# Performance work log

Measured on AMD Instinct MI355X. Metric: run time of the kernel, lower is better.

## Reference

```python
import jax, jax.numpy as jnp
import numpy as np

N_NODES = 100000
N_EDGES = 3200000
NUM_TYPES = 8
TYPE_DIM = 16
IN_DIM = 5
HID = 64
HEADS = 2
OUT = 64
LN_EPS = 1e-5
NEG_SLOPE = 0.2


def segment_softmax(logits, seg, num_segments):
    # logits: [E, H], seg: [E] destination ids
    m = jax.ops.segment_max(logits, seg, num_segments=num_segments)
    m = jnp.where(jnp.isfinite(m), m, 0.0)
    e = jnp.exp(logits - m[seg])
    s = jax.ops.segment_sum(e, seg, num_segments=num_segments)
    return e / (s[seg] + 1e-16)


def gat_conv(x, W, a_src, a_dst, b, src, dst, n_nodes, heads, ch):
    # x: [N, F_in], W: [F_in, heads*ch], a_src/a_dst: [heads, ch], b: [heads*ch]
    h = (x @ W).reshape(n_nodes, heads, ch)            # [N, H, C]
    al_s = jnp.einsum('nhc,hc->nh', h, a_src)          # [N, H]
    al_d = jnp.einsum('nhc,hc->nh', h, a_dst)          # [N, H]
    e = jax.nn.leaky_relu(al_s[src] + al_d[dst], NEG_SLOPE)  # [E, H]
    alpha = segment_softmax(e, dst, n_nodes)           # [E, H]
    msg = alpha[:, :, None] * h[src]                   # [E, H, C]
    out = jax.ops.segment_sum(msg, dst, num_segments=n_nodes)  # [N, H, C]
    return out.reshape(n_nodes, heads * ch) + b


def setup_inputs() -> dict:
    key = jax.random.key(0)
    ks = jax.random.split(key, 16)
    in1 = IN_DIM + TYPE_DIM  # 21
    inp = {
        'x': jax.random.normal(ks[0], (N_NODES, IN_DIM), dtype=jnp.float32),
        'edge_index': jax.random.randint(ks[1], (2, N_EDGES), 0, N_NODES, dtype=jnp.int32),
        'type_ids': jax.random.randint(ks[2], (N_NODES,), 0, NUM_TYPES, dtype=jnp.int32),
        'type_emb': jax.random.normal(ks[3], (NUM_TYPES, TYPE_DIM), dtype=jnp.float32) * 0.3,
        'W1': jax.random.normal(ks[4], (in1, HID), dtype=jnp.float32) * (1.0 / np.sqrt(in1)),
        'a_src1': jax.random.normal(ks[5], (HEADS, HID // HEADS), dtype=jnp.float32) * 0.1,
        'a_dst1': jax.random.normal(ks[6], (HEADS, HID // HEADS), dtype=jnp.float32) * 0.1,
        'b1': jnp.zeros((HID,), dtype=jnp.float32),
        'W2': jax.random.normal(ks[7], (HID, OUT), dtype=jnp.float32) * (1.0 / np.sqrt(HID)),
        'a_src2': jax.random.normal(ks[8], (1, OUT), dtype=jnp.float32) * 0.1,
        'a_dst2': jax.random.normal(ks[9], (1, OUT), dtype=jnp.float32) * 0.1,
        'b2': jnp.zeros((OUT,), dtype=jnp.float32),
        'gamma': jnp.ones((OUT,), dtype=jnp.float32),
        'beta': jnp.zeros((OUT,), dtype=jnp.float32),
    }
    return inp


def reference(x, type_emb, W1, a_src1, a_dst1, b1, W2, a_src2, a_dst2, b2, gamma, beta, edge_index, type_ids):
    n = x.shape[0]
    # type embedding concat
    xin = jnp.concatenate([x, type_emb[type_ids]], axis=1)  # [N, 21]
    # add self loops (PyG GATConv default)
    loops = jnp.arange(n, dtype=edge_index.dtype)
    src = jnp.concatenate([edge_index[0], loops])
    dst = jnp.concatenate([edge_index[1], loops])
    h = gat_conv(xin, W1, a_src1, a_dst1, b1, src, dst, n, HEADS, HID // HEADS)
    h = jax.nn.relu(h)  # dropout = identity at inference
    h = gat_conv(h, W2, a_src2, a_dst2, b2, src, dst, n, 1, OUT)
    # LayerNorm
    mu = jnp.mean(h, axis=-1, keepdims=True)
    var = jnp.var(h, axis=-1, keepdims=True)
    return (h - mu) / jnp.sqrt(var + LN_EPS) * gamma + beta
```

## Files before the change

### kernel.cpp

```cpp
#include <hip/hip_runtime.h>
#include <hip/hip_fp16.h>

#define NEG_SLOPE 0.2f
#define INVLN2 1.44269504088896f
#define BKT_SHIFT 7
#define BKT_NODES 128
#define BKT_CAP 5120
#define SRC_SHIFT 18
#define SRC_MASK 0x3FFFF
#define CHUNK 4096
#define NBMAX 1024

typedef _Float16 half8 __attribute__((ext_vector_type(8)));
typedef float float4v __attribute__((ext_vector_type(4)));

__global__ void k_bucketA(const int* __restrict__ ei, unsigned int* __restrict__ pk,
                          int* __restrict__ bcnt, int E, int NBKT)
{
    __shared__ unsigned int stage[CHUNK];
    __shared__ unsigned short stageB[CHUNK];
    __shared__ int cnt[NBMAX];
    __shared__ int excl[NBMAX];
    __shared__ int curp[NBMAX];
    __shared__ int gbase[NBMAX];

    int t = threadIdx.x;
    int e0 = blockIdx.x * CHUNK;
    bool vec4 = ((E & 3) == 0);

    for (int i = t; i < NBMAX; i += 256) cnt[i] = 0;
    __syncthreads();

    int4 s4[4], d4[4];
    bool val[4];

    if (vec4) {
#pragma unroll
        for (int it = 0; it < 4; it++) {
            int e = e0 + it * 1024 + t * 4;
            val[it] = (e < E);
            if (val[it]) {
                s4[it] = *(const int4*)(ei + e);
                d4[it] = *(const int4*)(ei + (size_t)E + e);
                atomicAdd(&cnt[d4[it].x >> BKT_SHIFT], 1);
                atomicAdd(&cnt[d4[it].y >> BKT_SHIFT], 1);
                atomicAdd(&cnt[d4[it].z >> BKT_SHIFT], 1);
                atomicAdd(&cnt[d4[it].w >> BKT_SHIFT], 1);
            }
        }
    } else {
        for (int i = t; i < CHUNK; i += 256) {
            int e = e0 + i;
            if (e >= E) break;
            atomicAdd(&cnt[ei[E + e] >> BKT_SHIFT], 1);
        }
    }
    __syncthreads();
    for (int i = t; i < NBMAX; i += 256) curp[i] = cnt[i];
    __syncthreads();
    for (int off = 1; off < NBMAX; off <<= 1) {
        int v0 = (t       >= off) ? cnt[t       - off] : 0;
        int v1 = (t + 256 >= off) ? cnt[t + 256 - off] : 0;
        int v2 = (t + 512 >= off) ? cnt[t + 512 - off] : 0;
        int v3 = (t + 768 >= off) ? cnt[t + 768 - off] : 0;
        __syncthreads();
        cnt[t] += v0; cnt[t + 256] += v1; cnt[t + 512] += v2; cnt[t + 768] += v3;
        __syncthreads();
    }
    for (int i = t; i < NBMAX; i += 256) {
        int o = curp[i];
        int ex = cnt[i] - o;
        excl[i] = ex;
        curp[i] = ex;
    }
    __syncthreads();
    for (int b = t; b < NBKT; b += 256) {
        int c = cnt[b] - excl[b];
        gbase[b] = (c > 0) ? atomicAdd(&bcnt[b], c) : 0;
    }
    __syncthreads();
    if (vec4) {
#pragma unroll
        for (int it = 0; it < 4; it++) {
            if (!val[it]) continue;
            int ss[4] = {s4[it].x, s4[it].y, s4[it].z, s4[it].w};
            int dd[4] = {d4[it].x, d4[it].y, d4[it].z, d4[it].w};
#pragma unroll
            for (int k = 0; k < 4; k++) {
                int b = dd[k] >> BKT_SHIFT;
                int p = atomicAdd(&curp[b], 1);
                stage[p] = (unsigned)ss[k] | ((unsigned)(dd[k] & (BKT_NODES - 1)) << SRC_SHIFT);
                stageB[p] = (unsigned short)b;
            }
        }
    } else {
        for (int i = t; i < CHUNK; i += 256) {
            int e = e0 + i;
            if (e >= E) break;
            int s = ei[e], d = ei[E + e];
            int b = d >> BKT_SHIFT;
            int p = atomicAdd(&curp[b], 1);
            stage[p] = (unsigned)s | ((unsigned)(d & (BKT_NODES - 1)) << SRC_SHIFT);
            stageB[p] = (unsigned short)b;
        }
    }
    __syncthreads();
    int total = E - e0; if (total > CHUNK) total = CHUNK;
    for (int i = t; i < total; i += 256) {
        int b = stageB[i];
        int idx = gbase[b] + (i - excl[b]);
        if (idx < BKT_CAP) pk[(size_t)b * BKT_CAP + idx] = stage[i];
    }
}

__global__ __launch_bounds__(256) void k_build_node1(
        const unsigned int* __restrict__ pk, const int* __restrict__ bcnt,
        int* __restrict__ rs, int* __restrict__ cur, int* __restrict__ ssrc,
        const float* __restrict__ x, const int* __restrict__ type_ids,
        const float* __restrict__ type_emb, const float* __restrict__ W1,
        const float* __restrict__ a_src1, const float* __restrict__ a_dst1,
        __half2* __restrict__ h1h, float* __restrict__ als1, float* __restrict__ ald1,
        int N, int NBKT)
{
    __shared__ unsigned int vals[BKT_CAP];
    __shared__ int cnt[BKT_NODES];
    __shared__ int cursor[BKT_NODES];
    __shared__ int orig[BKT_NODES];
    __shared__ int red[256];
    int t = threadIdx.x;

    if (blockIdx.x >= NBKT) {
        int node = (blockIdx.x - NBKT) * 4 + (t >> 6);
        int j = t & 63;
        if (node >= N) return;

        float xin[21];
#pragma unroll
        for (int k = 0; k < 5; k++) xin[k] = x[node * 5 + k];
        int ty = type_ids[node];
#pragma unroll
        for (int k = 0; k < 16; k++) xin[5 + k] = type_emb[ty * 16 + k];

        float h = 0.f;
#pragma unroll
        for (int k = 0; k < 21; k++) h += xin[k] * W1[k * 64 + j];

        float hn = __shfl_xor(h, 1);
        if ((j & 1) == 0)
            h1h[node * 32 + (j >> 1)] = __floats2half2_rn(h, hn);

        int head = j >> 5, lane = j & 31;
        float ps = h * a_src1[head * 32 + lane];
        float pd = h * a_dst1[head * 32 + lane];
#pragma unroll
        for (int m = 16; m >= 1; m >>= 1) { ps += __shfl_xor(ps, m); pd += __shfl_xor(pd, m); }
        if (lane == 0) {
            als1[node * 2 + head] = ps * INVLN2;
            ald1[node * 2 + head] = pd * INVLN2;
        }
        return;
    }

    int b = blockIdx.x;
    int nb = min(bcnt[b], BKT_CAP);

    int part = 0;
    for (int i = t; i < b; i += 256) part += min(bcnt[i], BKT_CAP);
    red[t] = part;
    if (t < BKT_NODES) cnt[t] = 0;
    __syncthreads();
    for (int off = 128; off; off >>= 1) {
        if (t < off) red[t] += red[t + off];
        __syncthreads();
    }
    int bs = red[0];

    const unsigned int* mypk = pk + (size_t)b * BKT_CAP;
    int nb4 = nb & ~3;
    for (int e = t * 4; e < nb4; e += 1024) {
        uint4 v = *(const uint4*)(mypk + e);
        *(uint4*)(vals + e) = v;
        atomicAdd(&cnt[v.x >> SRC_SHIFT], 1);
        atomicAdd(&cnt[v.y >> SRC_SHIFT], 1);
        atomicAdd(&cnt[v.z >> SRC_SHIFT], 1);
        atomicAdd(&cnt[v.w >> SRC_SHIFT], 1);
    }
    for (int e = nb4 + t; e < nb; e += 256) {
        unsigned int v = mypk[e];
        vals[e] = v;
        atomicAdd(&cnt[v >> SRC_SHIFT], 1);
    }
    __syncthreads();
    if (t < BKT_NODES) orig[t] = cnt[t];
    __syncthreads();
    for (int off = 1; off < BKT_NODES; off <<= 1) {
        int v = 0;
        if (t < BKT_NODES && t >= off) v = cnt[t - off];
        __syncthreads();
        if (t < BKT_NODES) cnt[t] += v;
        __syncthreads();
    }
    if (t < BKT_NODES) {
        int c = orig[t];
        int ex = cnt[t] - c;
        cursor[t] = ex;
        int node = (b << BKT_SHIFT) + t;
        if (node < N) { rs[node] = bs + ex; cur[node] = bs + ex + c; }
    }
    __syncthreads();
    for (int e = t; e < nb; e += 256) {
        unsigned int w = vals[e];
        int p = atomicAdd(&cursor[w >> SRC_SHIFT], 1);
        ssrc[bs + p] = (int)(w & SRC_MASK);
    }
}

__global__ void k_gather1(const int* __restrict__ rs, const int* __restrict__ cur,
                          const int* __restrict__ ssrc, const float4* __restrict__ h4,
                          const float* __restrict__ als1, const float* __restrict__ ald1,
                          const float* __restrict__ b1, float4* __restrict__ h2h4, int N)
{
    __shared__ int    sS[4][64];
    __shared__ float2 sW[4][64];
    int wv = threadIdx.x >> 6;
    int node = blockIdx.x * 4 + wv;
    if (node >= N) return;
    int l = threadIdx.x & 63;
    int eg = l >> 3;
    int ch = l & 7;
    int head = ch >> 2;
    float2 ad = ((const float2*)ald1)[node];

    int beg = rs[node], end = cur[node];
    int cnt = end - beg;
    const int* sp = ssrc + beg;
    __half2 acc2[4];
    acc2[0] = acc2[1] = acc2[2] = acc2[3] = __float2half2_rn(0.f);
    float ws0 = 0.f, ws1 = 0.f;

    for (int base = 0; base < cnt; base += 64) {
        int e = base + l;
        bool v = e < cnt;
        int s = v ? sp[e] : node;
        float2 al = ((const float2*)als1)[s];
        float lg0 = al.x + ad.x; lg0 = (lg0 >= 0.f) ? lg0 : NEG_SLOPE * lg0;
        float lg1 = al.y + ad.y; lg1 = (lg1 >= 0.f) ? lg1 : NEG_SLOPE * lg1;
        float w0 = v ? exp2f(lg0) : 0.f;
        float w1 = v ? exp2f(lg1) : 0.f;
        sS[wv][l] = s;
        sW[wv][l] = make_float2(w0, w1);
        ws0 += w0; ws1 += w1;

        int rem = cnt - base;
        const float* sWf = (const float*)&sW[wv][0];
        for (int sub = 0; sub < 8 && sub * 8 < rem; sub += 2) {
            int i0 = sub * 8 + eg, i1 = i0 + 8;
            int sA = sS[wv][i0];
            int sB = sS[wv][i1];
            float wA = sWf[i0 * 2 + head];
            float wB = sWf[i1 * 2 + head];
            float4 rA = h4[(size_t)sA * 8 + ch];
            float4 rB = h4[(size_t)sB * 8 + ch];
            __half2 whA = __float2half2_rn(wA);
            __half2 whB = __float2half2_rn(wB);
            const __half2* pA = (const __half2*)&rA;
            const __half2* pB = (const __half2*)&rB;
#pragma unroll
            for (int q = 0; q < 4; q++) {
                acc2[q] = __hfma2(pA[q], whA, acc2[q]);
                acc2[q] = __hfma2(pB[q], whB, acc2[q]);
            }
        }
    }
    float acc[8];
#pragma unroll
    for (int q = 0; q < 4; q++) {
        float2 f = __half22float2(acc2[q]);
        acc[2*q] = f.x; acc[2*q+1] = f.y;
    }
#pragma unroll
    for (int m = 1; m <= 32; m <<= 1) { ws0 += __shfl_xor(ws0, m); ws1 += __shfl_xor(ws1, m); }
#pragma unroll
    for (int m = 8; m <= 32; m <<= 1) {
#pragma unroll
        for (int q = 0; q < 8; q++) acc[q] += __shfl_xor(acc[q], m);
    }
    float wsum = head ? ws1 : ws0;
    {
        float2 al = ((const float2*)als1)[node];
        float lg = (head ? al.y + ad.y : al.x + ad.x);
        lg = (lg >= 0.f) ? lg : NEG_SLOPE * lg;
        float w = exp2f(lg);
        float4 r = h4[(size_t)node * 8 + ch];
        const __half2* p = (const __half2*)&r;
#pragma unroll
        for (int q = 0; q < 4; q++) {
            float2 f = __half22float2(p[q]);
            acc[2*q] += w * f.x; acc[2*q+1] += w * f.y;
        }
        wsum += w;
    }
    float inv = 1.f / (wsum + 1e-16f);
    if (eg == 0) {
        union { float4 f4; __half2 h2[4]; } u;
#pragma unroll
        for (int q = 0; q < 4; q++) {
            float v0 = fmaxf(acc[2*q]   * inv + b1[ch * 8 + 2*q],     0.f);
            float v1 = fmaxf(acc[2*q+1] * inv + b1[ch * 8 + 2*q + 1], 0.f);
            u.h2[q] = __floats2half2_rn(v0, v1);
        }
        h2h4[(size_t)node * 8 + ch] = u.f4;
    }
}

__global__ __launch_bounds__(256) void k_node2m(
        const _Float16* __restrict__ h2h, const float* __restrict__ W2,
        const float* __restrict__ a_src2, const float* __restrict__ a_dst2,
        _Float16* __restrict__ h3h, float* __restrict__ als2, float* __restrict__ ald2, int N)
{
    __shared__ _Float16 w2t[64][72];
    __shared__ float h3t[4][16][65];
    int t = threadIdx.x;
    for (int e = t; e < 4096; e += 256) {
        int k = e >> 6, n = e & 63;
        w2t[n][k] = (_Float16)W2[e];
    }
    __syncthreads();

    int w = t >> 6, l = t & 63;
    int l15 = l & 15, quad = l >> 4;
    int nodebase = blockIdx.x * 64 + w * 16;

    int arow = nodebase + l15;
    if (arow >= N) arow = N - 1;
    const half8* ap = (const half8*)(h2h + (size_t)arow * 64 + quad * 8);
    half8 a0 = ap[0];
    half8 a1 = ap[4];
    float4v accs[4];
#pragma unroll
    for (int nt = 0; nt < 4; nt++) {
        half8 b0 = *(const half8*)(&w2t[nt * 16 + l15][quad * 8]);
        half8 b1 = *(const half8*)(&w2t[nt * 16 + l15][32 + quad * 8]);
        float4v c = {0.f, 0.f, 0.f, 0.f};
        c = __builtin_amdgcn_mfma_f32_16x16x32_f16(a0, b0, c, 0, 0, 0);
        c = __builtin_amdgcn_mfma_f32_16x16x32_f16(a1, b1, c, 0, 0, 0);
        accs[nt] = c;
    }
#pragma unroll
    for (int nt = 0; nt < 4; nt++)
#pragma unroll
        for (int r = 0; r < 4; r++)
            h3t[w][quad * 4 + r][nt * 16 + l15] = accs[nt][r];
    __syncthreads();

    int m = l >> 2, part = l & 3;
    int g = blockIdx.x * 64 + w * 16 + m;
    float ps = 0.f, pd = 0.f;
    union { float4 f4[2]; _Float16 h[16]; } u;
#pragma unroll
    for (int c = 0; c < 16; c++) {
        float v = h3t[w][m][part * 16 + c];
        ps += v * a_src2[part * 16 + c];
        pd += v * a_dst2[part * 16 + c];
        u.h[c] = (_Float16)v;
    }
    if (g < N) {
        float4* dst = (float4*)(h3h + (size_t)g * 64) + part * 2;
        dst[0] = u.f4[0];
        dst[1] = u.f4[1];
    }
    ps += __shfl_xor(ps, 1); ps += __shfl_xor(ps, 2);
    pd += __shfl_xor(pd, 1); pd += __shfl_xor(pd, 2);
    if (part == 0 && g < N) { als2[g] = ps * INVLN2; ald2[g] = pd * INVLN2; }
}

__global__ void k_gather2(const int* __restrict__ rs, const int* __restrict__ cur,
                          const int* __restrict__ ssrc, const float4* __restrict__ h4,
                          const float* __restrict__ als2, const float* __restrict__ ald2,
                          const float* __restrict__ b2, const float* __restrict__ gamma,
                          const float* __restrict__ beta, float* __restrict__ out, int N)
{
    __shared__ int   sS[4][64];
    __shared__ float sW[4][64];
    int wv = threadIdx.x >> 6;
    int node = blockIdx.x * 4 + wv;
    if (node >= N) return;
    int l = threadIdx.x & 63;
    int eg = l >> 3;
    int ch = l & 7;
    float ad = ald2[node];

    int beg = rs[node], end = cur[node];
    int cnt = end - beg;
    const int* sp = ssrc + beg;
    __half2 acc2[4];
    acc2[0] = acc2[1] = acc2[2] = acc2[3] = __float2half2_rn(0.f);
    float ws = 0.f;

    for (int base = 0; base < cnt; base += 64) {
        int e = base + l;
        bool v = e < cnt;
        int s = v ? sp[e] : node;
        float lg = als2[s] + ad; lg = (lg >= 0.f) ? lg : NEG_SLOPE * lg;
        float w = v ? exp2f(lg) : 0.f;
        sS[wv][l] = s;
        sW[wv][l] = w;
        ws += w;

        int rem = cnt - base;
        for (int sub = 0; sub < 8 && sub * 8 < rem; sub += 2) {
            int i0 = sub * 8 + eg, i1 = i0 + 8;
            int sA = sS[wv][i0];
            int sB = sS[wv][i1];
            float wA = sW[wv][i0];
            float wB = sW[wv][i1];
            float4 rA = h4[(size_t)sA * 8 + ch];
            float4 rB = h4[(size_t)sB * 8 + ch];
            __half2 whA = __float2half2_rn(wA);
            __half2 whB = __float2half2_rn(wB);
            const __half2* pA = (const __half2*)&rA;
            const __half2* pB = (const __half2*)&rB;
#pragma unroll
            for (int q = 0; q < 4; q++) {
                acc2[q] = __hfma2(pA[q], whA, acc2[q]);
                acc2[q] = __hfma2(pB[q], whB, acc2[q]);
            }
        }
    }
    float acc[8];
#pragma unroll
    for (int q = 0; q < 4; q++) {
        float2 f = __half22float2(acc2[q]);
        acc[2*q] = f.x; acc[2*q+1] = f.y;
    }
#pragma unroll
    for (int m = 1; m <= 32; m <<= 1) ws += __shfl_xor(ws, m);
#pragma unroll
    for (int m = 8; m <= 32; m <<= 1) {
#pragma unroll
        for (int q = 0; q < 8; q++) acc[q] += __shfl_xor(acc[q], m);
    }
    {
        float lg = als2[node] + ad;
        lg = (lg >= 0.f) ? lg : NEG_SLOPE * lg;
        float w = exp2f(lg);
        float4 r = h4[(size_t)node * 8 + ch];
        const __half2* p = (const __half2*)&r;
#pragma unroll
        for (int q = 0; q < 4; q++) {
            float2 f = __half22float2(p[q]);
            acc[2*q] += w * f.x; acc[2*q+1] += w * f.y;
        }
        ws += w;
    }
    float inv = 1.f / (ws + 1e-16f);
    float o[8];
    float s = 0.f;
#pragma unroll
    for (int q = 0; q < 8; q++) { o[q] = acc[q] * inv + b2[ch * 8 + q]; s += o[q]; }
#pragma unroll
    for (int m = 1; m <= 4; m <<= 1) s += __shfl_xor(s, m);
    float mu = s * (1.f / 64.f);
    float v = 0.f;
#pragma unroll
    for (int q = 0; q < 8; q++) { float d = o[q] - mu; v += d * d; }
#pragma unroll
    for (int m = 1; m <= 4; m <<= 1) v += __shfl_xor(v, m);
    v *= (1.f / 64.f);
    float r = rsqrtf(v + 1e-5f);
    if (eg == 0) {
        float res[8];
#pragma unroll
        for (int q = 0; q < 8; q++)
            res[q] = (o[q] - mu) * r * gamma[ch * 8 + q] + beta[ch * 8 + q];
        float4* op = (float4*)(out + (size_t)node * 64 + ch * 8);
        op[0] = make_float4(res[0], res[1], res[2], res[3]);
        op[1] = make_float4(res[4], res[5], res[6], res[7]);
    }
}

extern "C" void kernel_launch(void* const* d_in, const int* in_sizes, int n_in,
                              void* d_out, int out_size, void* d_ws, size_t ws_size,
                              hipStream_t stream) {
    const float* x        = (const float*)d_in[0];
    const int*   ei       = (const int*)  d_in[1];
    const int*   type_ids = (const int*)  d_in[2];
    const float* type_emb = (const float*)d_in[3];
    const float* W1       = (const float*)d_in[4];
    const float* a_src1   = (const float*)d_in[5];
    const float* a_dst1   = (const float*)d_in[6];
    const float* b1       = (const float*)d_in[7];
    const float* W2       = (const float*)d_in[8];
    const float* a_src2   = (const float*)d_in[9];
    const float* a_dst2   = (const float*)d_in[10];
    const float* b2       = (const float*)d_in[11];
    const float* gamma    = (const float*)d_in[12];
    const float* beta     = (const float*)d_in[13];

    int N = in_sizes[0] / 5;
    int E = in_sizes[1] / 2;
    int NBKT = (N + BKT_NODES - 1) >> BKT_SHIFT;

    char* base = (char*)d_ws;
    size_t off = 0;
    auto carve = [&](size_t bytes) { void* p = base + off; off += (bytes + 255) & ~(size_t)255; return p; };
    __half2* h1h = (__half2*)carve((size_t)N * 64 * sizeof(__half));
    size_t pk_bytes = (size_t)NBKT * BKT_CAP * sizeof(unsigned int);
    size_t h23_bytes = 2 * (size_t)N * 64 * sizeof(__half);
    char* uni = (char*)carve(pk_bytes > h23_bytes ? pk_bytes : h23_bytes);
    _Float16* h2h = (_Float16*)uni;
    _Float16* h3h = (_Float16*)(uni + (size_t)N * 64 * sizeof(__half));
    unsigned int* pk = (unsigned int*)uni;
    float* als1  = (float*)carve((size_t)N * 2 * sizeof(float));
    float* ald1  = (float*)carve((size_t)N * 2 * sizeof(float));
    float* als2  = (float*)carve((size_t)N * sizeof(float));
    float* ald2  = (float*)carve((size_t)N * sizeof(float));
    int*   rs    = (int*)carve((size_t)N * sizeof(int));
    int*   cur   = (int*)carve((size_t)N * sizeof(int));
    int*   bcnt  = (int*)carve(1024 * sizeof(int));
    int*   ssrc  = (int*)carve((size_t)E * sizeof(int));

    dim3 tb(256);
    dim3 nb((N + 3) / 4);
    int nodeBlocks = (N + 3) / 4;

    hipMemsetAsync(bcnt, 0, NBKT * sizeof(int), stream);
    k_bucketA<<<dim3((E + CHUNK - 1) / CHUNK), tb, 0, stream>>>(ei, pk, bcnt, E, NBKT);

    k_build_node1<<<dim3(NBKT + nodeBlocks), tb, 0, stream>>>(
        pk, bcnt, rs, cur, ssrc,
        x, type_ids, type_emb, W1, a_src1, a_dst1, h1h, als1, ald1,
        N, NBKT);

    k_gather1<<<nb, tb, 0, stream>>>(rs, cur, ssrc, (const float4*)h1h, als1, ald1, b1,
                                     (float4*)h2h, N);
    k_node2m<<<dim3((N + 63) / 64), tb, 0, stream>>>(h2h, W2, a_src2, a_dst2,
                                                     h3h, als2, ald2, N);
    k_gather2<<<nb, tb, 0, stream>>>(rs, cur, ssrc, (const float4*)h3h, als2, ald2, b2,
                                     gamma, beta, (float*)d_out, N);
}
```

Baseline: 326.6 us.

## Split feature gathers into four channel-group planes for cache-resident gathers

Node feature tables are stored as four channel-group planes of 16 halves (32 bytes) each. Each gather kernel is launched with four blocks per node group, one per plane, so every gather pass works on a 3.2 MB working set that fits in L2, and each edge read fetches 32 bytes from one plane. LayerNorm moves into a separate kernel that reads a half-precision intermediate, because no single block now holds a full output row. In exchange, the edge index list and attention logits are reread four times, and there is an extra launch plus an intermediate round trip.

```diff
diff --git a/kernel.cpp b/kernel.cpp
--- a/kernel.cpp
+++ b/kernel.cpp
@@ -13,6 +13,12 @@
 
 typedef _Float16 half8 __attribute__((ext_vector_type(8)));
 typedef float float4v __attribute__((ext_vector_type(4)));
+
+static __device__ __forceinline__ __half2 shfl_xor_h2(__half2 v, int m) {
+    union { __half2 h; int i; } u; u.h = v;
+    u.i = __shfl_xor(u.i, m);
+    return u.h;
+}
 
 __global__ void k_bucketA(const int* __restrict__ ei, unsigned int* __restrict__ pk,
                           int* __restrict__ bcnt, int E, int NBKT)
@@ -119,7 +125,7 @@
         const float* __restrict__ x, const int* __restrict__ type_ids,
         const float* __restrict__ type_emb, const float* __restrict__ W1,
         const float* __restrict__ a_src1, const float* __restrict__ a_dst1,
-        __half2* __restrict__ h1h, float* __restrict__ als1, float* __restrict__ ald1,
+        __half2* __restrict__ h1t, float* __restrict__ als1, float* __restrict__ ald1,
         int N, int NBKT)
 {
     __shared__ unsigned int vals[BKT_CAP];
@@ -146,8 +152,11 @@
         for (int k = 0; k < 21; k++) h += xin[k] * W1[k * 64 + j];
 
         float hn = __shfl_xor(h, 1);
-        if ((j & 1) == 0)
-            h1h[node * 32 + (j >> 1)] = __floats2half2_rn(h, hn);
+        if ((j & 1) == 0) {
+            int g = j >> 4;
+            int idx = (j & 15) >> 1;
+            h1t[((size_t)g * N + node) * 8 + idx] = __floats2half2_rn(h, hn);
+        }
 
         int head = j >> 5, lane = j & 31;
         float ps = h * a_src1[head * 32 + lane];
@@ -215,101 +224,73 @@
     }
 }
 
-__global__ void k_gather1(const int* __restrict__ rs, const int* __restrict__ cur,
-                          const int* __restrict__ ssrc, const float4* __restrict__ h4,
-                          const float* __restrict__ als1, const float* __restrict__ ald1,
-                          const float* __restrict__ b1, float4* __restrict__ h2h4, int N)
+__global__ __launch_bounds__(256) void k_gatherg1(
+        const int* __restrict__ rs, const int* __restrict__ cur,
+        const int* __restrict__ ssrc, const float4* __restrict__ h1t,
+        const float* __restrict__ als1, const float* __restrict__ ald1,
+        const float* __restrict__ b1, float4* __restrict__ h2t, int N)
 {
-    __shared__ int    sS[4][64];
-    __shared__ float2 sW[4][64];
-    int wv = threadIdx.x >> 6;
-    int node = blockIdx.x * 4 + wv;
+    int g = blockIdx.x & 3;
+    int node = (blockIdx.x >> 2) * 4 + (threadIdx.x >> 6);
     if (node >= N) return;
     int l = threadIdx.x & 63;
-    int eg = l >> 3;
-    int ch = l & 7;
-    int head = ch >> 2;
-    float2 ad = ((const float2*)ald1)[node];
-
-    int beg = rs[node], end = cur[node];
-    int cnt = end - beg;
+    int eg = l >> 1, hf = l & 1;
+    int head = g >> 1;
+    float ad = ald1[node * 2 + head];
+
+    int beg = rs[node], cnt = cur[node] - beg;
     const int* sp = ssrc + beg;
     __half2 acc2[4];
     acc2[0] = acc2[1] = acc2[2] = acc2[3] = __float2half2_rn(0.f);
-    float ws0 = 0.f, ws1 = 0.f;
-
-    for (int base = 0; base < cnt; base += 64) {
-        int e = base + l;
+    float ws = 0.f;
+
+    for (int base = 0; base < cnt; base += 32) {
+        int e = base + eg;
         bool v = e < cnt;
         int s = v ? sp[e] : node;
-        float2 al = ((const float2*)als1)[s];
-        float lg0 = al.x + ad.x; lg0 = (lg0 >= 0.f) ? lg0 : NEG_SLOPE * lg0;
-        float lg1 = al.y + ad.y; lg1 = (lg1 >= 0.f) ? lg1 : NEG_SLOPE * lg1;
-        float w0 = v ? exp2f(lg0) : 0.f;
-        float w1 = v ? exp2f(lg1) : 0.f;
-        sS[wv][l] = s;
-        sW[wv][l] = make_float2(w0, w1);
-        ws0 += w0; ws1 += w1;
-
-        int rem = cnt - base;
-        const float* sWf = (const float*)&sW[wv][0];
-        for (int sub = 0; sub < 8 && sub * 8 < rem; sub += 2) {
-            int i0 = sub * 8 + eg, i1 = i0 + 8;
-            int sA = sS[wv][i0];
-            int sB = sS[wv][i1];
-            float wA = sWf[i0 * 2 + head];
-            float wB = sWf[i1 * 2 + head];
-            float4 rA = h4[(size_t)sA * 8 + ch];
-            float4 rB = h4[(size_t)sB * 8 + ch];
-            __half2 whA = __float2half2_rn(wA);
-            __half2 whB = __float2half2_rn(wB);
-            const __half2* pA = (const __half2*)&rA;
-            const __half2* pB = (const __half2*)&rB;
-#pragma unroll
-            for (int q = 0; q < 4; q++) {
-                acc2[q] = __hfma2(pA[q], whA, acc2[q]);
-                acc2[q] = __hfma2(pB[q], whB, acc2[q]);
-            }
-        }
-    }
+        float lg = als1[s * 2 + head] + ad;
+        lg = (lg >= 0.f) ? lg : NEG_SLOPE * lg;
+        float w = v ? exp2f(lg) : 0.f;
+        ws += w;
+        float4 r = h1t[((size_t)g * N + s) * 2 + hf];
+        __half2 wh = __float2half2_rn(w);
+        const __half2* p = (const __half2*)&r;
+#pragma unroll
+        for (int q = 0; q < 4; q++) acc2[q] = __hfma2(p[q], wh, acc2[q]);
+    }
+#pragma unroll
+    for (int m = 2; m <= 32; m <<= 1) {
+#pragma unroll
+        for (int q = 0; q < 4; q++) acc2[q] = __hadd2(acc2[q], shfl_xor_h2(acc2[q], m));
+    }
+#pragma unroll
+    for (int m = 1; m <= 32; m <<= 1) ws += __shfl_xor(ws, m);
+    ws *= 0.5f;
+
     float acc[8];
 #pragma unroll
-    for (int q = 0; q < 4; q++) {
-        float2 f = __half22float2(acc2[q]);
-        acc[2*q] = f.x; acc[2*q+1] = f.y;
-    }
-#pragma unroll
-    for (int m = 1; m <= 32; m <<= 1) { ws0 += __shfl_xor(ws0, m); ws1 += __shfl_xor(ws1, m); }
-#pragma unroll
-    for (int m = 8; m <= 32; m <<= 1) {
-#pragma unroll
-        for (int q = 0; q < 8; q++) acc[q] += __shfl_xor(acc[q], m);
-    }
-    float wsum = head ? ws1 : ws0;
+    for (int q = 0; q < 4; q++) { float2 f = __half22float2(acc2[q]); acc[2*q] = f.x; acc[2*q+1] = f.y; }
     {
-        float2 al = ((const float2*)als1)[node];
-        float lg = (head ? al.y + ad.y : al.x + ad.x);
+        float lg = als1[node * 2 + head] + ad;
         lg = (lg >= 0.f) ? lg : NEG_SLOPE * lg;
         float w = exp2f(lg);
-        float4 r = h4[(size_t)node * 8 + ch];
+        float4 r = h1t[((size_t)g * N + node) * 2 + hf];
         const __half2* p = (const __half2*)&r;
 #pragma unroll
+        for (int q = 0; q < 4; q++) { float2 f = __half22float2(p[q]); acc[2*q] += w * f.x; acc[2*q+1] += w * f.y; }
+        ws += w;
+    }
+    float inv = 1.f / (ws + 1e-16f);
+    if (eg == 0) {
+        const float* bb = b1 + g * 16 + hf * 8;
+        union { float4 f4; __half2 h2[4]; } u;
+#pragma unroll
         for (int q = 0; q < 4; q++) {
-            float2 f = __half22float2(p[q]);
-            acc[2*q] += w * f.x; acc[2*q+1] += w * f.y;
-        }
-        wsum += w;
-    }
-    float inv = 1.f / (wsum + 1e-16f);
-    if (eg == 0) {
-        union { float4 f4; __half2 h2[4]; } u;
-#pragma unroll
-        for (int q = 0; q < 4; q++) {
-            float v0 = fmaxf(acc[2*q]   * inv + b1[ch * 8 + 2*q],     0.f);
-            float v1 = fmaxf(acc[2*q+1] * inv + b1[ch * 8 + 2*q + 1], 0.f);
+            float v0 = fmaxf(acc[2*q]     * inv + bb[2*q],     0.f);
+            float v1 = fmaxf(acc[2*q + 1] * inv + bb[2*q + 1], 0.f);
             u.h2[q] = __floats2half2_rn(v0, v1);
         }
-        h2h4[(size_t)node * 8 + ch] = u.f4;
+        h2t[((size_t)g * N + node) * 2 + hf] = u.f4;
     }
 }
 
@@ -333,9 +314,10 @@
 
     int arow = nodebase + l15;
     if (arow >= N) arow = N - 1;
-    const half8* ap = (const half8*)(h2h + (size_t)arow * 64 + quad * 8);
-    half8 a0 = ap[0];
-    half8 a1 = ap[4];
+    const float4* h2t4 = (const float4*)h2h;
+    int g0 = quad >> 1, hf0 = quad & 1;
+    half8 a0 = *(const half8*)(h2t4 + ((size_t)g0 * N + arow) * 2 + hf0);
+    half8 a1 = *(const half8*)(h2t4 + ((size_t)(g0 + 2) * N + arow) * 2 + hf0);
     float4v accs[4];
 #pragma unroll
     for (int nt = 0; nt < 4; nt++) {
@@ -365,7 +347,7 @@
         u.h[c] = (_Float16)v;
     }
     if (g < N) {
-        float4* dst = (float4*)(h3h + (size_t)g * 64) + part * 2;
+        float4* dst = (float4*)h3h + ((size_t)part * N + g) * 2;
         dst[0] = u.f4[0];
         dst[1] = u.f4[1];
     }
@@ -374,109 +356,89 @@
     if (part == 0 && g < N) { als2[g] = ps * INVLN2; ald2[g] = pd * INVLN2; }
 }
 
-__global__ void k_gather2(const int* __restrict__ rs, const int* __restrict__ cur,
-                          const int* __restrict__ ssrc, const float4* __restrict__ h4,
-                          const float* __restrict__ als2, const float* __restrict__ ald2,
-                          const float* __restrict__ b2, const float* __restrict__ gamma,
-                          const float* __restrict__ beta, float* __restrict__ out, int N)
+__global__ __launch_bounds__(256) void k_gatherg2(
+        const int* __restrict__ rs, const int* __restrict__ cur,
+        const int* __restrict__ ssrc, const float4* __restrict__ h3t,
+        const float* __restrict__ als2, const float* __restrict__ ald2,
+        const float* __restrict__ b2, __half* __restrict__ ot, int N)
 {
-    __shared__ int   sS[4][64];
-    __shared__ float sW[4][64];
-    int wv = threadIdx.x >> 6;
-    int node = blockIdx.x * 4 + wv;
+    int g = blockIdx.x & 3;
+    int node = (blockIdx.x >> 2) * 4 + (threadIdx.x >> 6);
     if (node >= N) return;
     int l = threadIdx.x & 63;
-    int eg = l >> 3;
-    int ch = l & 7;
+    int eg = l >> 1, hf = l & 1;
     float ad = ald2[node];
 
-    int beg = rs[node], end = cur[node];
-    int cnt = end - beg;
+    int beg = rs[node], cnt = cur[node] - beg;
     const int* sp = ssrc + beg;
     __half2 acc2[4];
     acc2[0] = acc2[1] = acc2[2] = acc2[3] = __float2half2_rn(0.f);
     float ws = 0.f;
 
-    for (int base = 0; base < cnt; base += 64) {
-        int e = base + l;
+    for (int base = 0; base < cnt; base += 32) {
+        int e = base + eg;
         bool v = e < cnt;
         int s = v ? sp[e] : node;
-        float lg = als2[s] + ad; lg = (lg >= 0.f) ? lg : NEG_SLOPE * lg;
+        float lg = als2[s] + ad;
+        lg = (lg >= 0.f) ? lg : NEG_SLOPE * lg;
         float w = v ? exp2f(lg) : 0.f;
-        sS[wv][l] = s;
-        sW[wv][l] = w;
         ws += w;
-
-        int rem = cnt - base;
-        for (int sub = 0; sub < 8 && sub * 8 < rem; sub += 2) {
-            int i0 = sub * 8 + eg, i1 = i0 + 8;
-            int sA = sS[wv][i0];
-            int sB = sS[wv][i1];
-            float wA = sW[wv][i0];
-            float wB = sW[wv][i1];
-            float4 rA = h4[(size_t)sA * 8 + ch];
-            float4 rB = h4[(size_t)sB * 8 + ch];
-            __half2 whA = __float2half2_rn(wA);
-            __half2 whB = __float2half2_rn(wB);
-            const __half2* pA = (const __half2*)&rA;
-            const __half2* pB = (const __half2*)&rB;
-#pragma unroll
-            for (int q = 0; q < 4; q++) {
-                acc2[q] = __hfma2(pA[q], whA, acc2[q]);
-                acc2[q] = __hfma2(pB[q], whB, acc2[q]);
-            }
-        }
-    }
+        float4 r = h3t[((size_t)g * N + s) * 2 + hf];
+        __half2 wh = __float2half2_rn(w);
+        const __half2* p = (const __half2*)&r;
+#pragma unroll
+        for (int q = 0; q < 4; q++) acc2[q] = __hfma2(p[q], wh, acc2[q]);
+    }
+#pragma unroll
+    for (int m = 2; m <= 32; m <<= 1) {
+#pragma unroll
+        for (int q = 0; q < 4; q++) acc2[q] = __hadd2(acc2[q], shfl_xor_h2(acc2[q], m));
+    }
+#pragma unroll
+    for (int m = 1; m <= 32; m <<= 1) ws += __shfl_xor(ws, m);
+    ws *= 0.5f;
+
     float acc[8];
 #pragma unroll
-    for (int q = 0; q < 4; q++) {
-        float2 f = __half22float2(acc2[q]);
-        acc[2*q] = f.x; acc[2*q+1] = f.y;
-    }
-#pragma unroll
-    for (int m = 1; m <= 32; m <<= 1) ws += __shfl_xor(ws, m);
-#pragma unroll
-    for (int m = 8; m <= 32; m <<= 1) {
-#pragma unroll
-        for (int q = 0; q < 8; q++) acc[q] += __shfl_xor(acc[q], m);
-    }
+    for (int q = 0; q < 4; q++) { float2 f = __half22float2(acc2[q]); acc[2*q] = f.x; acc[2*q+1] = f.y; }
     {
         float lg = als2[node] + ad;
         lg = (lg >= 0.f) ? lg : NEG_SLOPE * lg;
         float w = exp2f(lg);
-        float4 r = h4[(size_t)node * 8 + ch];
+        float4 r = h3t[((size_t)g * N + node) * 2 + hf];
         const __half2* p = (const __half2*)&r;
 #pragma unroll
-        for (int q = 0; q < 4; q++) {
-            float2 f = __half22float2(p[q]);
-            acc[2*q] += w * f.x; acc[2*q+1] += w * f.y;
-        }
+        for (int q = 0; q < 4; q++) { float2 f = __half22float2(p[q]); acc[2*q] += w * f.x; acc[2*q+1] += w * f.y; }
         ws += w;
     }
     float inv = 1.f / (ws + 1e-16f);
-    float o[8];
-    float s = 0.f;
-#pragma unroll
-    for (int q = 0; q < 8; q++) { o[q] = acc[q] * inv + b2[ch * 8 + q]; s += o[q]; }
-#pragma unroll
-    for (int m = 1; m <= 4; m <<= 1) s += __shfl_xor(s, m);
+    if (eg == 0) {
+        const float* bb = b2 + g * 16 + hf * 8;
+        union { float4 f4; __half2 h2[4]; } u;
+#pragma unroll
+        for (int q = 0; q < 4; q++)
+            u.h2[q] = __floats2half2_rn(acc[2*q] * inv + bb[2*q], acc[2*q+1] * inv + bb[2*q+1]);
+        ((float4*)ot)[(size_t)node * 8 + g * 2 + hf] = u.f4;
+    }
+}
+
+__global__ void k_ln(const __half* __restrict__ ot, const float* __restrict__ gamma,
+                     const float* __restrict__ beta, float* __restrict__ out, int N)
+{
+    int node = blockIdx.x * 4 + (threadIdx.x >> 6);
+    if (node >= N) return;
+    int j = threadIdx.x & 63;
+    float o = __half2float(ot[(size_t)node * 64 + j]);
+    float s = o;
+#pragma unroll
+    for (int m = 1; m <= 32; m <<= 1) s += __shfl_xor(s, m);
     float mu = s * (1.f / 64.f);
-    float v = 0.f;
-#pragma unroll
-    for (int q = 0; q < 8; q++) { float d = o[q] - mu; v += d * d; }
-#pragma unroll
-    for (int m = 1; m <= 4; m <<= 1) v += __shfl_xor(v, m);
+    float d = o - mu;
+    float v = d * d;
+#pragma unroll
+    for (int m = 1; m <= 32; m <<= 1) v += __shfl_xor(v, m);
     v *= (1.f / 64.f);
-    float r = rsqrtf(v + 1e-5f);
-    if (eg == 0) {
-        float res[8];
-#pragma unroll
-        for (int q = 0; q < 8; q++)
-            res[q] = (o[q] - mu) * r * gamma[ch * 8 + q] + beta[ch * 8 + q];
-        float4* op = (float4*)(out + (size_t)node * 64 + ch * 8);
-        op[0] = make_float4(res[0], res[1], res[2], res[3]);
-        op[1] = make_float4(res[4], res[5], res[6], res[7]);
-    }
+    out[(size_t)node * 64 + j] = d * rsqrtf(v + 1e-5f) * gamma[j] + beta[j];
 }
 
 extern "C" void kernel_launch(void* const* d_in, const int* in_sizes, int n_in,
@@ -504,13 +466,14 @@
     char* base = (char*)d_ws;
     size_t off = 0;
     auto carve = [&](size_t bytes) { void* p = base + off; off += (bytes + 255) & ~(size_t)255; return p; };
-    __half2* h1h = (__half2*)carve((size_t)N * 64 * sizeof(__half));
+    __half2* h1t = (__half2*)carve((size_t)N * 64 * sizeof(__half));
     size_t pk_bytes = (size_t)NBKT * BKT_CAP * sizeof(unsigned int);
     size_t h23_bytes = 2 * (size_t)N * 64 * sizeof(__half);
     char* uni = (char*)carve(pk_bytes > h23_bytes ? pk_bytes : h23_bytes);
     _Float16* h2h = (_Float16*)uni;
     _Float16* h3h = (_Float16*)(uni + (size_t)N * 64 * sizeof(__half));
     unsigned int* pk = (unsigned int*)uni;
+    __half* ot = (__half*)h1t;
     float* als1  = (float*)carve((size_t)N * 2 * sizeof(float));
     float* ald1  = (float*)carve((size_t)N * 2 * sizeof(float));
     float* als2  = (float*)carve((size_t)N * sizeof(float));
@@ -521,21 +484,22 @@
     int*   ssrc  = (int*)carve((size_t)E * sizeof(int));
 
     dim3 tb(256);
-    dim3 nb((N + 3) / 4);
     int nodeBlocks = (N + 3) / 4;
+    dim3 gatherGrid(nodeBlocks * 4);
 
     hipMemsetAsync(bcnt, 0, NBKT * sizeof(int), stream);
     k_bucketA<<<dim3((E + CHUNK - 1) / CHUNK), tb, 0, stream>>>(ei, pk, bcnt, E, NBKT);
 
     k_build_node1<<<dim3(NBKT + nodeBlocks), tb, 0, stream>>>(
         pk, bcnt, rs, cur, ssrc,
-        x, type_ids, type_emb, W1, a_src1, a_dst1, h1h, als1, ald1,
+        x, type_ids, type_emb, W1, a_src1, a_dst1, h1t, als1, ald1,
         N, NBKT);
 
-    k_gather1<<<nb, tb, 0, stream>>>(rs, cur, ssrc, (const float4*)h1h, als1, ald1, b1,
-                                     (float4*)h2h, N);
+    k_gatherg1<<<gatherGrid, tb, 0, stream>>>(rs, cur, ssrc, (const float4*)h1t,
+                                              als1, ald1, b1, (float4*)h2h, N);
     k_node2m<<<dim3((N + 63) / 64), tb, 0, stream>>>(h2h, W2, a_src2, a_dst2,
                                                      h3h, als2, ald2, N);
-    k_gather2<<<nb, tb, 0, stream>>>(rs, cur, ssrc, (const float4*)h3h, als2, ald2, b2,
-                                     gamma, beta, (float*)d_out, N);
-}
+    k_gatherg2<<<gatherGrid, tb, 0, stream>>>(rs, cur, ssrc, (const float4*)h3h,
+                                              als2, ald2, b2, ot, N);
+    k_ln<<<dim3(nodeBlocks), tb, 0, stream>>>(ot, gamma, beta, (float*)d_out, N);
+}
```

Result: slower. 555.5 us (+70.1%).
